# Performance work log

Measured on AMD Instinct MI355X. Metric: run time of the kernel, lower is better.

## Reference

```python
import jax, jax.numpy as jnp
import numpy as np


def setup_inputs() -> dict:
    key = jax.random.key(0)
    k1, k2 = jax.random.split(key)
    n_tokens, embed_dim, num_embed = 16384, 512, 2048
    encode = jax.random.normal(k1, (n_tokens, embed_dim), dtype=jnp.float32)
    # Embedding init in torch: uniform(-1/num_embed, 1/num_embed)
    templat = jax.random.uniform(
        k2, (num_embed, embed_dim), dtype=jnp.float32,
        minval=-1.0 / num_embed, maxval=1.0 / num_embed)
    return {"encode": encode, "templat": templat}


def reference(encode, templat):
    # match_encode_with_templat, eval path: sample=False, detach='encode', metric='l2'
    encode_d = jax.lax.stop_gradient(encode)
    # squared L2 distance: ||e||^2 - 2 e@t^T + ||t||^2 ; logits = -dist
    e_sq = jnp.sum(encode_d * encode_d, axis=-1, keepdims=True)       # (N, 1)
    t_sq = jnp.sum(templat * templat, axis=-1)[None, :]               # (1, M)
    dist = e_sq - 2.0 * (encode_d @ templat.T) + t_sq                 # (N, M)
    logits = -dist
    zsoft = jax.nn.softmax(logits, axis=-1)
    zidx = jnp.argmax(zsoft, axis=-1)                                 # (N,)
    quant = templat[zidx]                                             # (N, C) gather
    return quant, zidx
```

## Files before the change

kernel.cpp:

```cpp
#include <hip/hip_runtime.h>
#include <stdint.h>

#define N_TOK  16384
#define EMB    512
#define NEMB   2048
#define NCHUNK 32
#define CWIN   2.5e-4f
#define WCAP   524288

typedef __attribute__((ext_vector_type(8))) short s16x8;
typedef __attribute__((ext_vector_type(4))) float f32x4;

__device__ __forceinline__ unsigned short f2bf(float f) {
  unsigned u = __float_as_uint(f);
  u += 0x7fffu + ((u >> 16) & 1u);
  return (unsigned short)(u >> 16);
}
__device__ __forceinline__ unsigned mapf(float f) {
  unsigned u = __float_as_uint(f);
  return (u >> 31) ? ~u : (u | 0x80000000u);
}
__device__ __forceinline__ float unmapf(unsigned u) {
  return __uint_as_float((u >> 31) ? (u & 0x7fffffffu) : ~u);
}

__device__ __forceinline__ float pairwise512_sq(const float* se, int lane) {
  int l = lane & 31;
  int b = l >> 3, j = l & 7;
  const float* base = se + b * 128 + j;
  float x = base[0];
  float r = __fmul_rn(x, x);
#pragma unroll
  for (int k = 1; k < 16; ++k) {
    float y = base[8 * k];
    r = __fadd_rn(r, __fmul_rn(y, y));
  }
  r = __fadd_rn(r, __shfl_xor(r, 1));
  r = __fadd_rn(r, __shfl_xor(r, 2));
  r = __fadd_rn(r, __shfl_xor(r, 4));
  r = __fadd_rn(r, __shfl_xor(r, 8));
  r = __fadd_rn(r, __shfl_xor(r, 16));
  return r;
}

__global__ __launch_bounds__(256) void prep_kernel(
    const float* __restrict__ tmp, const float* __restrict__ enc,
    unsigned short* __restrict__ thi, float* __restrict__ tsq,
    unsigned short* __restrict__ ehi, float* __restrict__ esq,
    int* __restrict__ wcount) {
  __shared__ float se[4][EMB];
  int wv = threadIdx.x >> 6, lane = threadIdx.x & 63;
  int row = blockIdx.x * 4 + wv;
  if (blockIdx.x == 0 && threadIdx.x == 0) *wcount = 0;
  bool isT = row < NEMB;
  const float* src = isT ? (tmp + (size_t)row * EMB)
                         : (enc + (size_t)(row - NEMB) * EMB);
  const float4* p = (const float4*)src + lane * 2;
  float4 v0 = p[0], v1 = p[1];
  float f[8] = {v0.x, v0.y, v0.z, v0.w, v1.x, v1.y, v1.z, v1.w};
  unsigned h[8];
#pragma unroll
  for (int i = 0; i < 8; ++i) { h[i] = f2bf(f[i]); se[wv][lane * 8 + i] = f[i]; }
  uint4 packed = { h[0] | (h[1] << 16), h[2] | (h[3] << 16),
                   h[4] | (h[5] << 16), h[6] | (h[7] << 16) };
  unsigned short* dsth = isT ? (thi + (size_t)row * EMB)
                             : (ehi + (size_t)(row - NEMB) * EMB);
  ((uint4*)dsth)[lane] = packed;
  __syncthreads();
  float s = pairwise512_sq(se[wv], lane);
  if (lane == 0) { if (isT) tsq[row] = s; else esq[row - NEMB] = s; }
}

__global__ __launch_bounds__(256, 3) void score_kernel(
    const unsigned short* __restrict__ ehi, const unsigned short* __restrict__ thi,
    const float* __restrict__ tsq,
    unsigned long long* __restrict__ keyc, unsigned* __restrict__ s2c) {
  __shared__ __align__(16) char smem[49152];
  const int tid = threadIdx.x, w = tid >> 6, lane = tid & 63;
  const int q = lane >> 4, r = lane & 15;
  const int wr = w >> 1, wc = w & 1;
  const int tokb = (int)blockIdx.x >> 4;
  const int nb   = (int)blockIdx.x & 15;

  const int Lp0 = w * 2048 + lane * 16;
  const int Lp1 = Lp0 + 1024;
  const int P0 = Lp0 ^ (((Lp0 >> 7) & 3) << 4);
  const int P1 = Lp1 ^ (((Lp1 >> 7) & 3) << 4);
  const int rw0 = P0 >> 6, cc0 = (P0 & 63) >> 1;
  const int rw1 = P1 >> 6, cc1 = (P1 & 63) >> 1;
  const unsigned short* paA0 = ehi + (size_t)(tokb * 128 + rw0) * EMB + cc0;
  const unsigned short* paA1 = ehi + (size_t)(tokb * 128 + rw1) * EMB + cc1;
  const unsigned short* pbB0 = thi + (size_t)(nb * 128 + rw0) * EMB + cc0;
  const unsigned short* pbB1 = thi + (size_t)(nb * 128 + rw1) * EMB + cc1;

#define GLD(src, dst)                                                    \
  __builtin_amdgcn_global_load_lds(                                      \
      (const __attribute__((address_space(1))) void*)(src),              \
      (__attribute__((address_space(3))) void*)(dst), 16, 0, 0)
#define STAGE(t) do {                                                    \
    char* da_ = smem + ((t) % 3) * 8192 + w * 2048;                      \
    char* db_ = smem + 24576 + ((t) % 3) * 8192 + w * 2048;              \
    GLD(paA0 + (t) * 32, da_);                                           \
    GLD(paA1 + (t) * 32, da_ + 1024);                                    \
    GLD(pbB0 + (t) * 32, db_);                                           \
    GLD(pbB1 + (t) * 32, db_ + 1024);                                    \
  } while (0)

  int offA[4], offB[4];
#pragma unroll
  for (int m = 0; m < 4; ++m) {
    int row = wr * 64 + m * 16 + r;
    int P = row * 64 + q * 16;
    offA[m] = P ^ (((P >> 7) & 3) << 4);
  }
#pragma unroll
  for (int n = 0; n < 4; ++n) {
    int row = wc * 64 + n * 16 + r;
    int P = row * 64 + q * 16;
    offB[n] = P ^ (((P >> 7) & 3) << 4);
  }

  f32x4 acc[4][4];
#pragma unroll
  for (int m = 0; m < 4; ++m)
#pragma unroll
    for (int n = 0; n < 4; ++n) acc[m][n] = (f32x4){0.f, 0.f, 0.f, 0.f};

  STAGE(0); STAGE(1);
  asm volatile("s_waitcnt vmcnt(4)" ::: "memory");
  __builtin_amdgcn_s_barrier();

#pragma unroll
  for (int t = 0; t < 16; ++t) {
    const char* Ab_ = smem + (t % 3) * 8192;
    const char* Bb_ = smem + 24576 + (t % 3) * 8192;
    if (t + 2 < 16) STAGE(t + 2);
    s16x8 af[4], bf[4];
#pragma unroll
    for (int m = 0; m < 4; ++m) af[m] = *(const s16x8*)(Ab_ + offA[m]);
#pragma unroll
    for (int n = 0; n < 4; ++n) bf[n] = *(const s16x8*)(Bb_ + offB[n]);
    __builtin_amdgcn_s_setprio(1);
#pragma unroll
    for (int n = 0; n < 4; ++n) {
      acc[0][n] = __builtin_amdgcn_mfma_f32_16x16x32_bf16(af[0], bf[n], acc[0][n], 0, 0, 0);
      acc[1][n] = __builtin_amdgcn_mfma_f32_16x16x32_bf16(af[1], bf[n], acc[1][n], 0, 0, 0);
      acc[2][n] = __builtin_amdgcn_mfma_f32_16x16x32_bf16(af[2], bf[n], acc[2][n], 0, 0, 0);
      acc[3][n] = __builtin_amdgcn_mfma_f32_16x16x32_bf16(af[3], bf[n], acc[3][n], 0, 0, 0);
    }
    __builtin_amdgcn_s_setprio(0);
    if (t < 14) { asm volatile("s_waitcnt vmcnt(4)" ::: "memory"); }
    else        { asm volatile("s_waitcnt vmcnt(0)" ::: "memory"); }
    __builtin_amdgcn_s_barrier();
  }

  const int chunk = nb * 2 + wc;
  const int nbase = chunk * 64;
  float tq[4];
#pragma unroll
  for (int n = 0; n < 4; ++n) tq[n] = tsq[nbase + n * 16 + r];
#pragma unroll
  for (int m = 0; m < 4; ++m) {
#pragma unroll
    for (int i = 0; i < 4; ++i) {
      unsigned long long k1 = ~0ULL; unsigned s2m = 0xffffffffu;
#pragma unroll
      for (int n = 0; n < 4; ++n) {
        float s = tq[n] - 2.0f * acc[m][n][i];
        unsigned sm = mapf(s);
        unsigned long long k =
            ((unsigned long long)sm << 32) | (unsigned)(nbase + n * 16 + r);
        if (k < k1) { unsigned o = (unsigned)(k1 >> 32); s2m = o < s2m ? o : s2m; k1 = k; }
        else s2m = sm < s2m ? sm : s2m;
      }
#pragma unroll
      for (int mask = 1; mask < 16; mask <<= 1) {
        unsigned long long ok = __shfl_xor(k1, mask);
        unsigned os = __shfl_xor(s2m, mask);
        if (ok < k1) { unsigned o = (unsigned)(k1 >> 32); s2m = o < s2m ? o : s2m; k1 = ok; }
        else { unsigned o = (unsigned)(ok >> 32); s2m = o < s2m ? o : s2m; }
        s2m = os < s2m ? os : s2m;
      }
      if (r == 0) {
        int token = tokb * 128 + wr * 64 + m * 16 + q * 4 + i;
        keyc[(size_t)chunk * N_TOK + token] = k1;
        s2c [(size_t)chunk * N_TOK + token] = s2m;
      }
    }
  }
#undef GLD
#undef STAGE
}

__global__ __launch_bounds__(256) void merge_kernel(
    const unsigned long long* __restrict__ keyc, const unsigned* __restrict__ s2c,
    int* __restrict__ bestIdx, int* __restrict__ flag, int* __restrict__ work,
    int* __restrict__ wcount, unsigned long long* __restrict__ rkey) {
  int t = blockIdx.x * 256 + threadIdx.x;
  if (t >= N_TOK) return;
  rkey[t] = ~0ULL;
  unsigned long long K = ~0ULL; unsigned S = 0xffffffffu;
  for (int c = 0; c < NCHUNK; ++c) {
    unsigned long long k = keyc[(size_t)c * N_TOK + t];
    unsigned s2 = s2c[(size_t)c * N_TOK + t];
    if (k < K) { unsigned o = (unsigned)(K >> 32); S = o < S ? o : S; K = k; }
    else { unsigned o = (unsigned)(k >> 32); S = o < S ? o : S; }
    S = s2 < S ? s2 : S;
  }
  float best_f   = unmapf((unsigned)(K >> 32));
  float second_f = unmapf(S);
  int idx = (int)(unsigned)(K & 0xffffffffu);
  bestIdx[t] = idx;
  bool ok = (second_f - best_f >= CWIN) && (idx >= 0) && (idx < NEMB) && (best_f == best_f);
  flag[t] = ok ? 0 : 1;
  if (!ok) {
    bool nanCase = !(best_f == best_f);
    float limit = best_f + CWIN;
    for (int c = 0; c < NCHUNK; ++c) {
      float cf = unmapf((unsigned)(keyc[(size_t)c * N_TOK + t] >> 32));
      if (nanCase || !(cf > limit)) {
        int pos = atomicAdd(wcount, 1);
        if (pos < WCAP) work[pos] = t * NCHUNK + c;
      }
    }
  }
}

__global__ __launch_bounds__(256) void refine_kernel(
    const float* __restrict__ enc, const float* __restrict__ tmp,
    const float* __restrict__ esq, const float* __restrict__ tsq,
    const int* __restrict__ work, const int* __restrict__ wcount,
    unsigned long long* __restrict__ rkey) {
  int total = *wcount; if (total > WCAP) total = WCAP;
  __shared__ float se[EMB];
  const int wv = threadIdx.x >> 6, lane = threadIdx.x & 63;
  const int g = lane >> 4, l16 = lane & 15;
  for (int p = blockIdx.x; p < total; p += gridDim.x) {
    __syncthreads();
    int item = work[p];
    int token = item / NCHUNK, c = item % NCHUNK;
    const float4* erow = (const float4*)(enc + (size_t)token * EMB);
    for (int i = threadIdx.x; i < 128; i += 256) ((float4*)se)[i] = erow[i];
    __syncthreads();
    float e2 = esq[token];
    unsigned long long lkey = ~0ULL;
#pragma unroll
    for (int j = 0; j < 4; ++j) {
      int m = c * 64 + wv * 16 + j * 4 + g;
      const float4* trow = (const float4*)(tmp + (size_t)m * EMB);
      double s = 0.0;
#pragma unroll
      for (int k = 0; k < 8; ++k) {
        float4 a = trow[l16 + 16 * k];
        float4 b = ((const float4*)se)[l16 + 16 * k];
        s += (double)a.x * b.x + (double)a.y * b.y
           + (double)a.z * b.z + (double)a.w * b.w;
      }
      s += __shfl_xor(s, 1); s += __shfl_xor(s, 2);
      s += __shfl_xor(s, 4); s += __shfl_xor(s, 8);
      if (l16 == 0) {
        float M  = (float)s;
        float d1 = __fadd_rn(e2, -__fmul_rn(2.0f, M));
        float d2 = __fadd_rn(d1, tsq[m]);
        unsigned long long key =
            ((unsigned long long)__float_as_uint(d2) << 32) | (unsigned)m;
        if (key < lkey) lkey = key;
      }
    }
    if (l16 == 0 && lkey != ~0ULL) atomicMin(&rkey[token], lkey);
  }
}

__global__ void gather_kernel(const float* __restrict__ tmp, const int* __restrict__ bestIdx,
                              const int* __restrict__ flag,
                              const unsigned long long* __restrict__ rkey,
                              float* __restrict__ out) {
  int token = blockIdx.x * 4 + (threadIdx.x >> 6);
  int lane = threadIdx.x & 63;
  int idx = flag[token] ? (int)(unsigned)(rkey[token] & 0xffffffffULL) : bestIdx[token];
  idx = idx < 0 ? 0 : (idx > NEMB - 1 ? NEMB - 1 : idx);
  const float4* src = (const float4*)(tmp + (size_t)idx * EMB) + lane * 2;
  float4* dst = (float4*)(out + (size_t)token * EMB) + lane * 2;
  dst[0] = src[0];
  dst[1] = src[1];
  if (lane == 0) out[(size_t)N_TOK * EMB + token] = (float)idx;
}

extern "C" void kernel_launch(void* const* d_in, const int* in_sizes, int n_in,
                              void* d_out, int out_size, void* d_ws, size_t ws_size,
                              hipStream_t stream) {
  const float* enc = (const float*)d_in[0];
  const float* tmp = (const float*)d_in[1];
  float* out = (float*)d_out;
  char* ws = (char*)d_ws;
  unsigned short* thi = (unsigned short*)ws;
  unsigned short* ehi = (unsigned short*)(ws + 2097152);
  float* tsq      = (float*)(ws + 18874368);
  float* esq      = (float*)(ws + 18882560);
  unsigned long long* keyc = (unsigned long long*)(ws + 18948096);
  unsigned* s2c   = (unsigned*)(ws + 23142400);
  int*   bestIdx  = (int*)  (ws + 25239552);
  int*   flag     = (int*)  (ws + 25305088);
  unsigned long long* rkey = (unsigned long long*)(ws + 25370624);
  int*   wcount   = (int*)  (ws + 25501696);
  int*   work     = (int*)  (ws + 25501760);

  prep_kernel  <<<4608,      256, 0, stream>>>(tmp, enc, thi, tsq, ehi, esq, wcount);
  score_kernel <<<2048,      256, 0, stream>>>(ehi, thi, tsq, keyc, s2c);
  merge_kernel <<<N_TOK/256, 256, 0, stream>>>(keyc, s2c, bestIdx, flag, work, wcount, rkey);
  refine_kernel<<<1024,      256, 0, stream>>>(enc, tmp, esq, tsq, work, wcount, rkey);
  gather_kernel<<<N_TOK/4,   256, 0, stream>>>(tmp, bestIdx, flag, rkey, out);
}
```

Baseline: 192.6 us.

## Widen score tile to 128x256 and store bf16 operands in k-tile-blocked layout

The prep kernel now writes the bf16 encode and template copies in a blocked layout: each 128-row block is split into 32-wide k-tiles, so one k-step of a tile is a contiguous 8 KB region. The score kernel's tile grows from 128x128 to 128x256 codebook entries, with 4x8 MFMA accumulators per wave and a larger triple-buffered LDS B buffer. The grid is halved and each block writes two chunks of argmin/second-min results. The intent is more operand reuse per LDS load and more contiguous global-to-LDS copies. The cost is more registers and LDS, and occupancy drops from 3 to 2 blocks per CU.

```diff
diff --git a/kernel.cpp b/kernel.cpp
--- a/kernel.cpp
+++ b/kernel.cpp
@@ -63,128 +63,140 @@
   for (int i = 0; i < 8; ++i) { h[i] = f2bf(f[i]); se[wv][lane * 8 + i] = f[i]; }
   uint4 packed = { h[0] | (h[1] << 16), h[2] | (h[3] << 16),
                    h[4] | (h[5] << 16), h[6] | (h[7] << 16) };
-  unsigned short* dsth = isT ? (thi + (size_t)row * EMB)
-                             : (ehi + (size_t)(row - NEMB) * EMB);
-  ((uint4*)dsth)[lane] = packed;
+  int lrow = isT ? row : row - NEMB;
+  int blk = lrow >> 7, lr = lrow & 127;
+  int kt = lane >> 2, cb = (lane & 3) * 16;
+  char* base = (char*)(isT ? thi : ehi);
+  *(uint4*)(base + (((size_t)(blk * 16 + kt)) << 13) + lr * 64 + cb) = packed;
   __syncthreads();
   float s = pairwise512_sq(se[wv], lane);
   if (lane == 0) { if (isT) tsq[row] = s; else esq[row - NEMB] = s; }
 }
 
-__global__ __launch_bounds__(256, 3) void score_kernel(
+__global__ __launch_bounds__(256, 2) void score_kernel(
     const unsigned short* __restrict__ ehi, const unsigned short* __restrict__ thi,
     const float* __restrict__ tsq,
     unsigned long long* __restrict__ keyc, unsigned* __restrict__ s2c) {
-  __shared__ __align__(16) char smem[49152];
+  __shared__ __align__(16) char smem[73728];
   const int tid = threadIdx.x, w = tid >> 6, lane = tid & 63;
   const int q = lane >> 4, r = lane & 15;
   const int wr = w >> 1, wc = w & 1;
-  const int tokb = (int)blockIdx.x >> 4;
-  const int nb   = (int)blockIdx.x & 15;
-
-  const int Lp0 = w * 2048 + lane * 16;
-  const int Lp1 = Lp0 + 1024;
-  const int P0 = Lp0 ^ (((Lp0 >> 7) & 3) << 4);
-  const int P1 = Lp1 ^ (((Lp1 >> 7) & 3) << 4);
-  const int rw0 = P0 >> 6, cc0 = (P0 & 63) >> 1;
-  const int rw1 = P1 >> 6, cc1 = (P1 & 63) >> 1;
-  const unsigned short* paA0 = ehi + (size_t)(tokb * 128 + rw0) * EMB + cc0;
-  const unsigned short* paA1 = ehi + (size_t)(tokb * 128 + rw1) * EMB + cc1;
-  const unsigned short* pbB0 = thi + (size_t)(nb * 128 + rw0) * EMB + cc0;
-  const unsigned short* pbB1 = thi + (size_t)(nb * 128 + rw1) * EMB + cc1;
+  const int tokb = (int)blockIdx.x >> 3;
+  const int nbp  = (int)blockIdx.x & 7;
+
+  const unsigned short* paA[2];
+  const unsigned short* pbB[4];
+#pragma unroll
+  for (int i = 0; i < 2; ++i) {
+    int Lp = i * 4096 + tid * 16;
+    int P = Lp ^ (((Lp >> 7) & 3) << 4);
+    paA[i] = (const unsigned short*)((const char*)ehi
+             + (((size_t)tokb * 16) << 13) + (P >> 6) * 64 + (P & 63));
+  }
+#pragma unroll
+  for (int i = 0; i < 4; ++i) {
+    int Lp = i * 4096 + tid * 16;
+    int P = Lp ^ (((Lp >> 7) & 3) << 4);
+    int sub = P >> 13, rw = (P >> 6) & 127, cbyte = P & 63;
+    pbB[i] = (const unsigned short*)((const char*)thi
+             + (((size_t)((nbp * 2 + sub) * 16)) << 13) + rw * 64 + cbyte);
+  }
 
 #define GLD(src, dst)                                                    \
   __builtin_amdgcn_global_load_lds(                                      \
       (const __attribute__((address_space(1))) void*)(src),              \
       (__attribute__((address_space(3))) void*)(dst), 16, 0, 0)
 #define STAGE(t) do {                                                    \
-    char* da_ = smem + ((t) % 3) * 8192 + w * 2048;                      \
-    char* db_ = smem + 24576 + ((t) % 3) * 8192 + w * 2048;              \
-    GLD(paA0 + (t) * 32, da_);                                           \
-    GLD(paA1 + (t) * 32, da_ + 1024);                                    \
-    GLD(pbB0 + (t) * 32, db_);                                           \
-    GLD(pbB1 + (t) * 32, db_ + 1024);                                    \
+    char* da_ = smem + ((t) % 3) * 8192 + tid * 16;                      \
+    char* db_ = smem + 24576 + ((t) % 3) * 16384 + tid * 16;             \
+    GLD((const char*)paA[0] + (size_t)(t) * 8192, da_);                  \
+    GLD((const char*)paA[1] + (size_t)(t) * 8192, da_ + 4096);           \
+    GLD((const char*)pbB[0] + (size_t)(t) * 8192, db_);                  \
+    GLD((const char*)pbB[1] + (size_t)(t) * 8192, db_ + 4096);           \
+    GLD((const char*)pbB[2] + (size_t)(t) * 8192, db_ + 8192);           \
+    GLD((const char*)pbB[3] + (size_t)(t) * 8192, db_ + 12288);          \
   } while (0)
 
-  int offA[4], offB[4];
+  int offA[4], offB[8];
 #pragma unroll
   for (int m = 0; m < 4; ++m) {
-    int row = wr * 64 + m * 16 + r;
-    int P = row * 64 + q * 16;
+    int P = (wr * 64 + m * 16 + r) * 64 + q * 16;
     offA[m] = P ^ (((P >> 7) & 3) << 4);
   }
 #pragma unroll
-  for (int n = 0; n < 4; ++n) {
-    int row = wc * 64 + n * 16 + r;
-    int P = row * 64 + q * 16;
+  for (int n = 0; n < 8; ++n) {
+    int P = (wc * 128 + n * 16 + r) * 64 + q * 16;
     offB[n] = P ^ (((P >> 7) & 3) << 4);
   }
 
-  f32x4 acc[4][4];
+  f32x4 acc[4][8];
 #pragma unroll
   for (int m = 0; m < 4; ++m)
 #pragma unroll
-    for (int n = 0; n < 4; ++n) acc[m][n] = (f32x4){0.f, 0.f, 0.f, 0.f};
+    for (int n = 0; n < 8; ++n) acc[m][n] = (f32x4){0.f, 0.f, 0.f, 0.f};
 
   STAGE(0); STAGE(1);
-  asm volatile("s_waitcnt vmcnt(4)" ::: "memory");
+  asm volatile("s_waitcnt vmcnt(6)" ::: "memory");
   __builtin_amdgcn_s_barrier();
 
 #pragma unroll
   for (int t = 0; t < 16; ++t) {
     const char* Ab_ = smem + (t % 3) * 8192;
-    const char* Bb_ = smem + 24576 + (t % 3) * 8192;
+    const char* Bb_ = smem + 24576 + (t % 3) * 16384;
     if (t + 2 < 16) STAGE(t + 2);
-    s16x8 af[4], bf[4];
+    s16x8 af[4], bf[8];
 #pragma unroll
     for (int m = 0; m < 4; ++m) af[m] = *(const s16x8*)(Ab_ + offA[m]);
 #pragma unroll
-    for (int n = 0; n < 4; ++n) bf[n] = *(const s16x8*)(Bb_ + offB[n]);
+    for (int n = 0; n < 8; ++n) bf[n] = *(const s16x8*)(Bb_ + offB[n]);
     __builtin_amdgcn_s_setprio(1);
 #pragma unroll
-    for (int n = 0; n < 4; ++n) {
+    for (int n = 0; n < 8; ++n) {
       acc[0][n] = __builtin_amdgcn_mfma_f32_16x16x32_bf16(af[0], bf[n], acc[0][n], 0, 0, 0);
       acc[1][n] = __builtin_amdgcn_mfma_f32_16x16x32_bf16(af[1], bf[n], acc[1][n], 0, 0, 0);
       acc[2][n] = __builtin_amdgcn_mfma_f32_16x16x32_bf16(af[2], bf[n], acc[2][n], 0, 0, 0);
       acc[3][n] = __builtin_amdgcn_mfma_f32_16x16x32_bf16(af[3], bf[n], acc[3][n], 0, 0, 0);
     }
     __builtin_amdgcn_s_setprio(0);
-    if (t < 14) { asm volatile("s_waitcnt vmcnt(4)" ::: "memory"); }
+    if (t < 14) { asm volatile("s_waitcnt vmcnt(6)" ::: "memory"); }
     else        { asm volatile("s_waitcnt vmcnt(0)" ::: "memory"); }
     __builtin_amdgcn_s_barrier();
   }
 
-  const int chunk = nb * 2 + wc;
-  const int nbase = chunk * 64;
-  float tq[4];
-#pragma unroll
-  for (int n = 0; n < 4; ++n) tq[n] = tsq[nbase + n * 16 + r];
-#pragma unroll
-  for (int m = 0; m < 4; ++m) {
-#pragma unroll
-    for (int i = 0; i < 4; ++i) {
-      unsigned long long k1 = ~0ULL; unsigned s2m = 0xffffffffu;
-#pragma unroll
-      for (int n = 0; n < 4; ++n) {
-        float s = tq[n] - 2.0f * acc[m][n][i];
-        unsigned sm = mapf(s);
-        unsigned long long k =
-            ((unsigned long long)sm << 32) | (unsigned)(nbase + n * 16 + r);
-        if (k < k1) { unsigned o = (unsigned)(k1 >> 32); s2m = o < s2m ? o : s2m; k1 = k; }
-        else s2m = sm < s2m ? sm : s2m;
-      }
-#pragma unroll
-      for (int mask = 1; mask < 16; mask <<= 1) {
-        unsigned long long ok = __shfl_xor(k1, mask);
-        unsigned os = __shfl_xor(s2m, mask);
-        if (ok < k1) { unsigned o = (unsigned)(k1 >> 32); s2m = o < s2m ? o : s2m; k1 = ok; }
-        else { unsigned o = (unsigned)(ok >> 32); s2m = o < s2m ? o : s2m; }
-        s2m = os < s2m ? os : s2m;
-      }
-      if (r == 0) {
-        int token = tokb * 128 + wr * 64 + m * 16 + q * 4 + i;
-        keyc[(size_t)chunk * N_TOK + token] = k1;
-        s2c [(size_t)chunk * N_TOK + token] = s2m;
+#pragma unroll
+  for (int nh = 0; nh < 2; ++nh) {
+    const int chunk = nbp * 4 + wc * 2 + nh;
+    const int nbase = chunk * 64;
+    float tq[4];
+#pragma unroll
+    for (int nn = 0; nn < 4; ++nn) tq[nn] = tsq[nbase + nn * 16 + r];
+#pragma unroll
+    for (int m = 0; m < 4; ++m) {
+#pragma unroll
+      for (int i = 0; i < 4; ++i) {
+        unsigned long long k1 = ~0ULL; unsigned s2m = 0xffffffffu;
+#pragma unroll
+        for (int nn = 0; nn < 4; ++nn) {
+          float s = tq[nn] - 2.0f * acc[m][nh * 4 + nn][i];
+          unsigned sm = mapf(s);
+          unsigned long long k =
+              ((unsigned long long)sm << 32) | (unsigned)(nbase + nn * 16 + r);
+          if (k < k1) { unsigned o = (unsigned)(k1 >> 32); s2m = o < s2m ? o : s2m; k1 = k; }
+          else s2m = sm < s2m ? sm : s2m;
+        }
+#pragma unroll
+        for (int mask = 1; mask < 16; mask <<= 1) {
+          unsigned long long ok = __shfl_xor(k1, mask);
+          unsigned os = __shfl_xor(s2m, mask);
+          if (ok < k1) { unsigned o = (unsigned)(k1 >> 32); s2m = o < s2m ? o : s2m; k1 = ok; }
+          else { unsigned o = (unsigned)(ok >> 32); s2m = o < s2m ? o : s2m; }
+          s2m = os < s2m ? os : s2m;
+        }
+        if (r == 0) {
+          int token = tokb * 128 + wr * 64 + m * 16 + q * 4 + i;
+          keyc[(size_t)chunk * N_TOK + token] = k1;
+          s2c [(size_t)chunk * N_TOK + token] = s2m;
+        }
       }
     }
   }
@@ -306,7 +318,7 @@
   int*   work     = (int*)  (ws + 25501760);
 
   prep_kernel  <<<4608,      256, 0, stream>>>(tmp, enc, thi, tsq, ehi, esq, wcount);
-  score_kernel <<<2048,      256, 0, stream>>>(ehi, thi, tsq, keyc, s2c);
+  score_kernel <<<1024,      256, 0, stream>>>(ehi, thi, tsq, keyc, s2c);
   merge_kernel <<<N_TOK/256, 256, 0, stream>>>(keyc, s2c, bestIdx, flag, work, wcount, rkey);
   refine_kernel<<<1024,      256, 0, stream>>>(enc, tmp, esq, tsq, work, wcount, rkey);
   gather_kernel<<<N_TOK/4,   256, 0, stream>>>(tmp, bestIdx, flag, rkey, out);
```

Result: slower. 198.5 us (+3.1%).
